# Kernel tuning notes

Measured on AMD Instinct MI355X. Metric: run time of the kernel, lower is better.

## Reference

```python
import jax, jax.numpy as jnp
import numpy as np

B, S, E, H = 2, 2048, 1024, 16
D = E // H  # head_dim
SCALE = 1.0 / np.sqrt(D)


def rope_tables(seq_len, dim, dtype=jnp.float32):
    # matches RotaryEmbedding: inv_freq over even indices, emb = cat([freqs, freqs])
    inv_freq = 1.0 / (10000.0 ** (jnp.arange(0, dim, 2, dtype=dtype) / dim))
    t = jnp.arange(seq_len, dtype=dtype)
    freqs = t[:, None] * inv_freq[None, :]          # [S, D/2]
    emb = jnp.concatenate([freqs, freqs], axis=-1)  # [S, D]
    return jnp.cos(emb)[None, None], jnp.sin(emb)[None, None]  # [1,1,S,D]


def apply_rope(x, cos, sin):
    # x: [B,H,S,D]; interleaved rotate exactly as the torch code:
    # x2 = stack([-x[...,1::2], x[...,0::2]], -1).reshape_as(x)
    x2 = jnp.stack([-x[..., 1::2], x[..., 0::2]], axis=-1).reshape(x.shape)
    return x * cos + x2 * sin


def setup_inputs() -> dict:
    key = jax.random.key(0)
    ks = jax.random.split(key, 12)
    std = 1.0 / np.sqrt(E)
    inp = {
        "query": jax.random.normal(ks[0], (B, S, E), jnp.float32),
        "key": jax.random.normal(ks[1], (B, S, E), jnp.float32),
        "value": jax.random.normal(ks[2], (B, S, E), jnp.float32),
        "mask": jnp.ones((B, S), jnp.int32),
        "Wq": jax.random.normal(ks[3], (E, E), jnp.float32) * std,
        "bq": jax.random.normal(ks[4], (E,), jnp.float32) * std,
        "Wk": jax.random.normal(ks[5], (E, E), jnp.float32) * std,
        "bk": jax.random.normal(ks[6], (E,), jnp.float32) * std,
        "Wv": jax.random.normal(ks[7], (E, E), jnp.float32) * std,
        "bv": jax.random.normal(ks[8], (E,), jnp.float32) * std,
        "Wo": jax.random.normal(ks[9], (E, E), jnp.float32) * std,
        "bo": jax.random.normal(ks[10], (E,), jnp.float32) * std,
    }
    return inp


def reference(query, key, value, mask, Wq, bq, Wk, bk, Wv, bv, Wo, bo):
    b, sq, _ = query.shape
    sk = key.shape[1]
    # linear projections (torch Linear: x @ W.T + b), split into heads [B,H,S,D]
    Q = (query @ Wq.T + bq).reshape(b, sq, H, D).transpose(0, 2, 1, 3)
    K = (key @ Wk.T + bk).reshape(b, sk, H, D).transpose(0, 2, 1, 3)
    V = (value @ Wv.T + bv).reshape(b, sk, H, D).transpose(0, 2, 1, 3)
    cos_q, sin_q = rope_tables(sq, D)
    cos_k, sin_k = rope_tables(sk, D)
    Q = apply_rope(Q, cos_q, sin_q)
    K = apply_rope(K, cos_k, sin_k)
    scores = jnp.einsum("bhqd,bhkd->bhqk", Q, K) * SCALE
    neg_inf = jnp.finfo(scores.dtype).min
    scores = jnp.where(mask[:, None, None, :] == 0, neg_inf, scores)
    attn = jax.nn.softmax(scores, axis=-1)
    # dropout omitted (deterministic reference / eval mode)
    out = jnp.einsum("bhqk,bhkd->bhqd", attn, V)
    out = out.transpose(0, 2, 1, 3).reshape(b, sq, E)
    return out @ Wo.T + bo
```

## Files before the change

### kernel.cpp

```cpp
#include <hip/hip_runtime.h>
#include <stdint.h>

typedef unsigned short u16;
typedef __bf16 bf16x8 __attribute__((ext_vector_type(8)));
typedef float f32x4 __attribute__((ext_vector_type(4)));
typedef float f32x2 __attribute__((ext_vector_type(2)));
typedef u16 u16x4v __attribute__((ext_vector_type(4)));

#define DI __device__ __forceinline__

constexpr int BB = 2, SS = 2048, EE = 1024, HH = 16, DD = 64;
constexpr int MROWS = BB * SS;
constexpr int KDIM = 1024, NDIM = 1024;

constexpr float FM = 12.0f;
constexpr float MNEG = -30000.f;

DI u16 f2bf(float f) {
  uint32_t u = __float_as_uint(f);
  return (u16)((u + 0x7FFFu + ((u >> 16) & 1u)) >> 16);
}
DI float bf2f(u16 h) { return __uint_as_float(((uint32_t)h) << 16); }

DI uint32_t cvtpk_bf16(float a, float b) {
  uint32_t r;
  asm("v_cvt_pk_bf16_f32 %0, %1, %2" : "=v"(r) : "v"(a), "v"(b));
  return r;
}

DI void cp16(const void* g, void* lds) {
  __builtin_amdgcn_global_load_lds((const __attribute__((address_space(1))) void*)g,
                                   (__attribute__((address_space(3))) void*)lds, 16, 0, 0);
}

DI f32x4 mfma16(bf16x8 a, bf16x8 b, f32x4 c) {
  return __builtin_amdgcn_mfma_f32_16x16x32_bf16(a, b, c, 0, 0, 0);
}

__global__ __launch_bounds__(256) void prep_cast(
    const float* __restrict__ q, const float* __restrict__ k, const float* __restrict__ v,
    const float* __restrict__ wq, const float* __restrict__ wk, const float* __restrict__ wv,
    const float* __restrict__ wo, const int* __restrict__ mask,
    u16* __restrict__ qb, u16* __restrict__ kb, u16* __restrict__ vb,
    u16* __restrict__ wqb, u16* __restrict__ wkb, u16* __restrict__ wvb,
    u16* __restrict__ wob, float* __restrict__ csT, float* __restrict__ mfl) {
  constexpr size_t SZI = (size_t)MROWS * EE;
  constexpr size_t SZW = (size_t)EE * EE;
  const int t = blockIdx.x * 256 + threadIdx.x;
  if (t < SS * 64) {
    const int s = t >> 6, d = t & 63, j = d & 31;
    const float ang = (float)s * exp2f(-(float)j * 0.4152410118f);
    float2 cs; cs.x = cosf(ang); cs.y = sinf(ang);
    ((float2*)csT)[t] = cs;
    if (t < BB * SS) mfl[t] = mask[t] ? -FM : MNEG;
  }
  const size_t g = ((size_t)blockIdx.x * 256 + threadIdx.x) * 4;
  const float* src; u16* dst; size_t o;
  if (g < SZI)          { src = q; dst = qb; o = g; }
  else if (g < 2 * SZI) { src = k; dst = kb; o = g - SZI; }
  else if (g < 3 * SZI) { src = v; dst = vb; o = g - 2 * SZI; }
  else {
    size_t t2 = g - 3 * SZI;
    int wi = (int)(t2 / SZW);
    o = t2 - (size_t)(wi < 4 ? wi : 3) * SZW;
    src = wi == 0 ? wq : wi == 1 ? wk : wi == 2 ? wv : wo;
    dst = wi == 0 ? wqb : wi == 1 ? wkb : wi == 2 ? wvb : wob;
  }
  const float4 f = *(const float4*)(src + o);
  u16x4v hv;
  hv[0] = f2bf(f.x); hv[1] = f2bf(f.y); hv[2] = f2bf(f.z); hv[3] = f2bf(f.w);
  *(u16x4v*)(dst + o) = hv;
}

__global__ __launch_bounds__(256) void gemm_qkv(
    const u16* __restrict__ qb, const u16* __restrict__ kb, const u16* __restrict__ vb,
    const u16* __restrict__ wqb, const u16* __restrict__ wkb, const u16* __restrict__ wvb,
    const float* __restrict__ bq, const float* __restrict__ bk, const float* __restrict__ bv,
    u16* __restrict__ Qp, u16* __restrict__ Kp, u16* __restrict__ Vtg,
    const float* __restrict__ csT) {
  __shared__ alignas(16) u16 sA[2][128 * 64];
  __shared__ alignas(16) u16 sB[2][128 * 64];
  const int flat = blockIdx.y * 8 + blockIdx.x;
  const int swz = (flat & 7) * 96 + (flat >> 3);
  const int bx = swz & 7, by = swz >> 3;

  const int tsel = by >> 5;
  const bool vtr = (tsel == 2);
  const u16* A    = tsel == 0 ? wqb : tsel == 1 ? wkb : vb;
  const u16* Bm   = tsel == 0 ? qb  : tsel == 1 ? kb  : wvb;
  const float* bias = tsel == 0 ? bq : tsel == 1 ? bk : bv;

  const int fBase = bx * 128;
  const int tBase = (by & 31) * 128;
  const int aBase = vtr ? tBase : fBase;
  const int bBase = vtr ? fBase : tBase;
  const int tid = threadIdx.x;
  const int lane = tid & 63, w = tid >> 6;
  const int quad = lane >> 4, l16 = lane & 15;
  const int wr = w >> 1, wc = w & 1;

  size_t aSrc[4], bSrc[4];
  int dOff[4];
#pragma unroll
  for (int j = 0; j < 4; ++j) {
    const int c = tid + j * 256;
    const int row = c >> 3, sl = c & 7;
    const size_t off = (size_t)row * KDIM + ((sl ^ (row & 7)) * 8);
    aSrc[j] = (size_t)aBase * KDIM + off;
    bSrc[j] = (size_t)bBase * KDIM + off;
    dOff[j] = c * 8;
  }

  f32x4 acc[4][4];
#pragma unroll
  for (int mi = 0; mi < 4; ++mi)
#pragma unroll
    for (int ni = 0; ni < 4; ++ni)
#pragma unroll
      for (int e = 0; e < 4; ++e) acc[mi][ni][e] = 0.f;

  const int arow = wr * 64 + l16, brow = wc * 64 + l16;

  auto stage = [&](int k0, int bi) {
#pragma unroll
    for (int j = 0; j < 4; ++j) {
      cp16(A + aSrc[j] + k0, &sA[bi][dOff[j]]);
      cp16(Bm + bSrc[j] + k0, &sB[bi][dOff[j]]);
    }
  };

  stage(0, 0);
  __syncthreads();
  int buf = 0;
  for (int k0 = 0; k0 < KDIM; k0 += 64) {
    if (k0 + 64 < KDIM) stage(k0 + 64, buf ^ 1);
    __builtin_amdgcn_s_setprio(1);
#pragma unroll
    for (int h = 0; h < 2; ++h) {
      bf16x8 af[4], bf[4];
#pragma unroll
      for (int i = 0; i < 4; ++i) {
        const int ar = arow + i * 16, br = brow + i * 16;
        af[i] = *(const bf16x8*)&sA[buf][ar * 64 + (((h * 4 + quad) ^ (ar & 7)) << 3)];
        bf[i] = *(const bf16x8*)&sB[buf][br * 64 + (((h * 4 + quad) ^ (br & 7)) << 3)];
      }
#pragma unroll
      for (int mi = 0; mi < 4; ++mi)
#pragma unroll
        for (int ni = 0; ni < 4; ++ni)
          acc[mi][ni] = mfma16(af[mi], bf[ni], acc[mi][ni]);
    }
    __builtin_amdgcn_s_setprio(0);
    __syncthreads();
    buf ^= 1;
  }

  if (!vtr) {
    u16* C = tsel == 0 ? Qp : Kp;
#pragma unroll
    for (int mi = 0; mi < 4; ++mi) {
      const int fm = fBase + wr * 64 + mi * 16 + quad * 4;
      const float4 b4 = *(const float4*)&bias[fm];
      const int d0 = fm & 63;
#pragma unroll
      for (int ni = 0; ni < 4; ++ni) {
        const int t = tBase + wc * 64 + ni * 16 + l16;
        const int srow = t & (SS - 1);
        const float* cs = &csT[(size_t)((srow << 6) + d0) * 2];
        const float4 cs01 = *(const float4*)cs;
        const float4 cs23 = *(const float4*)(cs + 4);
        const float v0 = acc[mi][ni][0] + b4.x;
        const float v1 = acc[mi][ni][1] + b4.y;
        const float v2 = acc[mi][ni][2] + b4.z;
        const float v3 = acc[mi][ni][3] + b4.w;
        const float o0 = v0 * cs01.x - v1 * cs01.y;
        const float o1 = v1 * cs01.z + v0 * cs01.w;
        const float o2 = v2 * cs23.x - v3 * cs23.y;
        const float o3 = v3 * cs23.z + v2 * cs23.w;
        uint2 pk;
        pk.x = cvtpk_bf16(o0, o1);
        pk.y = cvtpk_bf16(o2, o3);
        *(uint2*)&C[(size_t)t * NDIM + fm] = pk;
      }
    }
  } else {
#pragma unroll
    for (int ni = 0; ni < 4; ++ni) {
      const int f = fBase + wc * 64 + ni * 16 + l16;
      const int h = f >> 6, d = f & 63;
      const float bb = bias[f];
#pragma unroll
      for (int mi = 0; mi < 4; ++mi) {
        const int t0 = tBase + wr * 64 + mi * 16 + quad * 4;
        const int b = t0 >> 11, s0 = t0 & (SS - 1);
        const int sp0 = (s0 & ~31) | (((s0 >> 2) & 3) << 3) | (((s0 >> 4) & 1) << 2);
        uint2 pk;
        pk.x = cvtpk_bf16(acc[mi][ni][0] + bb, acc[mi][ni][1] + bb);
        pk.y = cvtpk_bf16(acc[mi][ni][2] + bb, acc[mi][ni][3] + bb);
        *(uint2*)&Vtg[((size_t)((b * 16 + h) * 64 + d)) * SS + sp0] = pk;
      }
    }
  }
}

__global__ __launch_bounds__(512, 4) void attn_kernel(
    const u16* __restrict__ Qp, const u16* __restrict__ Kp, const u16* __restrict__ Vtg,
    const float* __restrict__ mfl, u16* __restrict__ Oh) {
  __shared__ alignas(16) u16 sm[36864];
  const int flat = blockIdx.y * 16 + blockIdx.x;
  const int swz = (flat & 7) * 64 + (flat >> 3);
  const int bqx = swz & 15, bh = swz >> 4;

  const int tid = threadIdx.x, lane = tid & 63, w = tid >> 6;
  const int quad = lane >> 4, l16 = lane & 15;
  const int b = bh >> 4, h = bh & 15;
  const int q0 = bqx * 128 + (w & 3) * 32;
  const int grp = w >> 2, wl = w & 3;
  const u16* Qb = Qp + (size_t)b * SS * EE + h * DD;
  const u16* Kb = Kp + (size_t)b * SS * EE + h * DD;
  const u16* Vb = Vtg + (size_t)bh * DD * SS;
  constexpr float C1 = 0.18033688011112042f;
  float* smask = (float*)&sm[32768];

  bf16x8 qf[2][2];
#pragma unroll
  for (int qi = 0; qi < 2; ++qi)
#pragma unroll
    for (int ks = 0; ks < 2; ++ks)
      qf[qi][ks] = *(const bf16x8*)(Qb + (size_t)(q0 + qi * 16 + l16) * EE + ks * 32 + quad * 8);

  f32x4 oacc[2][4];
#pragma unroll
  for (int qi = 0; qi < 2; ++qi)
#pragma unroll
    for (int nd = 0; nd < 4; ++nd)
#pragma unroll
      for (int e = 0; e < 4; ++e) oacc[qi][nd][e] = 0.f;
  f32x2 sum2[2];
  sum2[0] = {0.f, 0.f}; sum2[1] = {0.f, 0.f};

  const int gtid = tid & 255;

  auto stage = [&](int w_, int bi) {
    const int key0 = w_ * 128 + grp * 64;
    u16* dK = &sm[grp * 16384 + bi * 4096];
    u16* dV = &sm[grp * 16384 + 8192 + bi * 4096];
#pragma unroll
    for (int i = 0; i < 2; ++i) {
      const int c = i * 256 + gtid;
      const int key = c >> 3, sl = c & 7;
      cp16(Kb + (size_t)(key0 + key) * EE + ((sl ^ (key & 7)) * 8), &dK[c * 8]);
    }
#pragma unroll
    for (int i = 0; i < 2; ++i) {
      const int c = i * 256 + gtid;
      const int d = c >> 3, sl = c & 7;
      cp16(Vb + (size_t)d * SS + key0 + ((sl ^ (d & 7)) * 8), &dV[c * 8]);
    }
  };

  auto compute = [&](int w_, int bi) {
    const int key0 = w_ * 128 + grp * 64;
    const u16* sK_ = &sm[grp * 16384 + bi * 4096];
    const u16* sV_ = &sm[grp * 16384 + 8192 + bi * 4096];
    f32x4 sacc[2][4];
#pragma unroll
    for (int qi = 0; qi < 2; ++qi)
#pragma unroll
      for (int ni = 0; ni < 4; ++ni)
#pragma unroll
        for (int e = 0; e < 4; ++e) sacc[qi][ni][e] = 0.f;
    __builtin_amdgcn_s_setprio(1);
#pragma unroll
    for (int ks = 0; ks < 2; ++ks)
#pragma unroll
      for (int ni = 0; ni < 4; ++ni) {
        const int row = ni * 16 + l16;
        const bf16x8 kf = *(const bf16x8*)&sK_[row * 64 + (((ks * 4 + quad) ^ (l16 & 7)) << 3)];
#pragma unroll
        for (int qi = 0; qi < 2; ++qi)
          sacc[qi][ni] = mfma16(kf, qf[qi][ks], sacc[qi][ni]);
      }
    __builtin_amdgcn_s_setprio(0);

    f32x2 mh01[4], mh23[4];
#pragma unroll
    for (int ni = 0; ni < 4; ++ni) {
      const int kb4 = key0 + ni * 16 + quad * 4;
      mh01[ni] = *(const f32x2*)&smask[kb4];
      mh23[ni] = *(const f32x2*)&smask[kb4 + 2];
    }

    uint32_t pw32[2][2][4];
#pragma unroll
    for (int qi = 0; qi < 2; ++qi)
#pragma unroll
      for (int ni = 0; ni < 4; ++ni) {
        f32x2 t01, t23;
        t01.x = sacc[qi][ni][0]; t01.y = sacc[qi][ni][1];
        t23.x = sacc[qi][ni][2]; t23.y = sacc[qi][ni][3];
        t01 = t01 * C1 + mh01[ni];
        t23 = t23 * C1 + mh23[ni];
        f32x2 p01, p23;
        p01.x = __builtin_amdgcn_exp2f(t01.x); p01.y = __builtin_amdgcn_exp2f(t01.y);
        p23.x = __builtin_amdgcn_exp2f(t23.x); p23.y = __builtin_amdgcn_exp2f(t23.y);
        sum2[qi] += p01;
        sum2[qi] += p23;
        const int k2 = ni >> 1, j2 = (ni & 1) * 2;
        pw32[qi][k2][j2]     = cvtpk_bf16(p01.x, p01.y);
        pw32[qi][k2][j2 + 1] = cvtpk_bf16(p23.x, p23.y);
      }

    __builtin_amdgcn_s_setprio(1);
#pragma unroll
    for (int k2 = 0; k2 < 2; ++k2) {
      union { uint32_t u[4]; bf16x8 v; } pf[2];
#pragma unroll
      for (int qi = 0; qi < 2; ++qi)
#pragma unroll
        for (int j = 0; j < 4; ++j) pf[qi].u[j] = pw32[qi][k2][j];
#pragma unroll
      for (int nd = 0; nd < 4; ++nd) {
        const int row = nd * 16 + l16;
        const bf16x8 vf = *(const bf16x8*)&sV_[row * 64 + (((k2 * 4 + quad) ^ (l16 & 7)) << 3)];
#pragma unroll
        for (int qi = 0; qi < 2; ++qi)
          oacc[qi][nd] = mfma16(pf[qi].v, vf, oacc[qi][nd]);
      }
    }
    __builtin_amdgcn_s_setprio(0);
  };

  stage(0, 0);
  cp16(mfl + (size_t)b * SS + tid * 4, &sm[32768 + tid * 8]);
  __syncthreads();

  for (int w_ = 0; w_ < 16; ++w_) {
    if (w_ + 1 < 16) stage(w_ + 1, (w_ + 1) & 1);
    compute(w_, w_ & 1);
    __syncthreads();
  }

  float lg[2];
#pragma unroll
  for (int qi = 0; qi < 2; ++qi) {
    float s = sum2[qi].x + sum2[qi].y;
    s += __shfl_xor(s, 16, 64);
    s += __shfl_xor(s, 32, 64);
    lg[qi] = s;
  }

  float* sO = (float*)&sm[0];
  float* l0 = smask;
  if (grp == 0) {
#pragma unroll
    for (int qi = 0; qi < 2; ++qi)
#pragma unroll
      for (int nd = 0; nd < 4; ++nd)
#pragma unroll
        for (int e = 0; e < 4; ++e) {
          const int q = wl * 32 + qi * 16 + quad * 4 + e;
          sO[q * 65 + nd * 16 + l16] = oacc[qi][nd][e];
        }
    if (quad == 0) {
      l0[wl * 32 + l16] = lg[0];
      l0[wl * 32 + 16 + l16] = lg[1];
    }
  }
  __syncthreads();
  if (grp == 1) {
    float linv[2];
#pragma unroll
    for (int qi = 0; qi < 2; ++qi) {
      const float lt = l0[wl * 32 + qi * 16 + l16] + lg[qi];
      linv[qi] = lt > 0.f ? 1.0f / lt : 0.f;
    }
#pragma unroll
    for (int qi = 0; qi < 2; ++qi)
#pragma unroll
      for (int r = 0; r < 4; ++r) {
        const float li = __shfl(linv[qi], quad * 4 + r, 16);
        const int q = wl * 32 + qi * 16 + quad * 4 + r;
        const size_t row = (size_t)(b * SS + bqx * 128 + q) * EE + h * DD;
#pragma unroll
        for (int nd = 0; nd < 4; ++nd) {
          const int d = nd * 16 + l16;
          Oh[row + d] = f2bf((sO[q * 65 + d] + oacc[qi][nd][r]) * li);
        }
      }
  }
}

__global__ __launch_bounds__(256) void gemm_out(
    const u16* __restrict__ Ab, const u16* __restrict__ Bb,
    const float* __restrict__ bias, float* __restrict__ Cout) {
  __shared__ alignas(16) u16 sA[2][128 * 64];
  __shared__ alignas(16) u16 sB[2][64 * 64];
  const int flat = blockIdx.y * 16 + blockIdx.x;
  const int swz = (flat & 7) * 64 + (flat >> 3);
  const int bx = swz & 15, by = swz >> 4;

  const int rowBase = by * 128;
  const int colBase = bx * 64;
  const int tid = threadIdx.x;
  const int lane = tid & 63, w = tid >> 6;
  const int quad = lane >> 4, l16 = lane & 15;
  const int wr = w >> 1, wc = w & 1;

  size_t aSrc[4]; int aOff[4];
  size_t bSrc[2]; int bOff[2];
#pragma unroll
  for (int j = 0; j < 4; ++j) {
    const int c = tid + j * 256;
    const int row = c >> 3, sl = c & 7;
    aSrc[j] = (size_t)(rowBase + row) * KDIM + ((sl ^ (row & 7)) * 8);
    aOff[j] = c * 8;
  }
#pragma unroll
  for (int j = 0; j < 2; ++j) {
    const int c = tid + j * 256;
    const int row = c >> 3, sl = c & 7;
    bSrc[j] = (size_t)(colBase + row) * KDIM + ((sl ^ (row & 7)) * 8);
    bOff[j] = c * 8;
  }

  f32x4 acc[4][2];
#pragma unroll
  for (int mi = 0; mi < 4; ++mi)
#pragma unroll
    for (int ni = 0; ni < 2; ++ni)
#pragma unroll
      for (int e = 0; e < 4; ++e) acc[mi][ni][e] = 0.f;

  const int arow = wr * 64 + l16, brow = wc * 32 + l16;

  auto stage = [&](int k0, int bi) {
#pragma unroll
    for (int j = 0; j < 4; ++j) cp16(Ab + aSrc[j] + k0, &sA[bi][aOff[j]]);
#pragma unroll
    for (int j = 0; j < 2; ++j) cp16(Bb + bSrc[j] + k0, &sB[bi][bOff[j]]);
  };

  stage(0, 0);
  __syncthreads();
  int buf = 0;
  for (int k0 = 0; k0 < KDIM; k0 += 64) {
    if (k0 + 64 < KDIM) stage(k0 + 64, buf ^ 1);
    __builtin_amdgcn_s_setprio(1);
#pragma unroll
    for (int h = 0; h < 2; ++h) {
      bf16x8 af[4], bf[2];
#pragma unroll
      for (int i = 0; i < 4; ++i) {
        const int ar = arow + i * 16;
        af[i] = *(const bf16x8*)&sA[buf][ar * 64 + (((h * 4 + quad) ^ (ar & 7)) << 3)];
      }
#pragma unroll
      for (int i = 0; i < 2; ++i) {
        const int br = brow + i * 16;
        bf[i] = *(const bf16x8*)&sB[buf][br * 64 + (((h * 4 + quad) ^ (br & 7)) << 3)];
      }
#pragma unroll
      for (int mi = 0; mi < 4; ++mi)
#pragma unroll
        for (int ni = 0; ni < 2; ++ni)
          acc[mi][ni] = mfma16(af[mi], bf[ni], acc[mi][ni]);
    }
    __builtin_amdgcn_s_setprio(0);
    __syncthreads();
    buf ^= 1;
  }

#pragma unroll
  for (int mi = 0; mi < 4; ++mi) {
    const int rb = rowBase + wr * 64 + mi * 16 + quad * 4;
#pragma unroll
    for (int ni = 0; ni < 2; ++ni) {
      const int col = colBase + wc * 32 + ni * 16 + l16;
      const float bb = bias[col];
#pragma unroll
      for (int r = 0; r < 4; ++r)
        Cout[(size_t)(rb + r) * NDIM + col] = acc[mi][ni][r] + bb;
    }
  }
}

extern "C" void kernel_launch(void* const* d_in, const int* in_sizes, int n_in,
                              void* d_out, int out_size, void* d_ws, size_t ws_size,
                              hipStream_t stream) {
  const float* q    = (const float*)d_in[0];
  const float* k    = (const float*)d_in[1];
  const float* v    = (const float*)d_in[2];
  const int*   mask = (const int*)d_in[3];
  const float* Wq = (const float*)d_in[4];
  const float* bq = (const float*)d_in[5];
  const float* Wk = (const float*)d_in[6];
  const float* bk = (const float*)d_in[7];
  const float* Wv = (const float*)d_in[8];
  const float* bv = (const float*)d_in[9];
  const float* Wo = (const float*)d_in[10];
  const float* bo = (const float*)d_in[11];
  float* out = (float*)d_out;
  char* ws = (char*)d_ws;
  constexpr size_t MB = 1024 * 1024;
  u16* qb  = (u16*)(ws + 0 * MB);
  u16* kb  = (u16*)(ws + 8 * MB);
  u16* vb  = (u16*)(ws + 16 * MB);
  u16* wqb = (u16*)(ws + 24 * MB);
  u16* wkb = (u16*)(ws + 26 * MB);
  u16* wvb = (u16*)(ws + 28 * MB);
  u16* wob = (u16*)(ws + 30 * MB);
  u16* Qp  = (u16*)(ws + 32 * MB);
  u16* Kp  = (u16*)(ws + 40 * MB);
  u16* Vtg = (u16*)(ws + 48 * MB);
  u16* oh  = (u16*)(ws + 56 * MB);
  float* csT = (float*)(ws + 64 * MB);
  float* mfl = out;

  prep_cast<<<16384, 256, 0, stream>>>(q, k, v, Wq, Wk, Wv, Wo, mask,
                                       qb, kb, vb, wqb, wkb, wvb, wob, csT, mfl);
  gemm_qkv<<<dim3(8, 96), 256, 0, stream>>>(qb, kb, vb, wqb, wkb, wvb,
                                            bq, bk, bv, Qp, Kp, Vtg, csT);
  attn_kernel<<<dim3(16, 32), 512, 0, stream>>>(Qp, Kp, Vtg, mfl, oh);
  gemm_out<<<dim3(16, 32), 256, 0, stream>>>(oh, wob, bo, out);
}
```

Baseline: 217.2 us.

## Fuse fp32-to-bf16 activation cast into QKV GEMM loads

The prep kernel now casts only the weights and builds the RoPE and mask tables. The fp32 activation casts move into gemm_qkv, which loads fp32 query/key/value tiles into registers, converts them with v_cvt_pk_bf16, and writes them to LDS after the MFMA phase, while weights still use async global-to-LDS copies. This drops a full write and reread of the three bf16 activation copies. In exchange the GEMM reads twice the activation bytes per tile, needs more registers, and does register-staged LDS writes on the critical path.

```diff
diff --git a/kernel.cpp b/kernel.cpp
--- a/kernel.cpp
+++ b/kernel.cpp
@@ -20,7 +20,6 @@
   uint32_t u = __float_as_uint(f);
   return (u16)((u + 0x7FFFu + ((u >> 16) & 1u)) >> 16);
 }
-DI float bf2f(u16 h) { return __uint_as_float(((uint32_t)h) << 16); }
 
 DI uint32_t cvtpk_bf16(float a, float b) {
   uint32_t r;
@@ -37,15 +36,12 @@
   return __builtin_amdgcn_mfma_f32_16x16x32_bf16(a, b, c, 0, 0, 0);
 }
 
-__global__ __launch_bounds__(256) void prep_cast(
-    const float* __restrict__ q, const float* __restrict__ k, const float* __restrict__ v,
-    const float* __restrict__ wq, const float* __restrict__ wk, const float* __restrict__ wv,
-    const float* __restrict__ wo, const int* __restrict__ mask,
-    u16* __restrict__ qb, u16* __restrict__ kb, u16* __restrict__ vb,
+__global__ __launch_bounds__(256) void prep_w(
+    const float* __restrict__ wq, const float* __restrict__ wk,
+    const float* __restrict__ wv, const float* __restrict__ wo,
+    const int* __restrict__ mask,
     u16* __restrict__ wqb, u16* __restrict__ wkb, u16* __restrict__ wvb,
     u16* __restrict__ wob, float* __restrict__ csT, float* __restrict__ mfl) {
-  constexpr size_t SZI = (size_t)MROWS * EE;
-  constexpr size_t SZW = (size_t)EE * EE;
   const int t = blockIdx.x * 256 + threadIdx.x;
   if (t < SS * 64) {
     const int s = t >> 6, d = t & 63, j = d & 31;
@@ -54,18 +50,11 @@
     ((float2*)csT)[t] = cs;
     if (t < BB * SS) mfl[t] = mask[t] ? -FM : MNEG;
   }
-  const size_t g = ((size_t)blockIdx.x * 256 + threadIdx.x) * 4;
-  const float* src; u16* dst; size_t o;
-  if (g < SZI)          { src = q; dst = qb; o = g; }
-  else if (g < 2 * SZI) { src = k; dst = kb; o = g - SZI; }
-  else if (g < 3 * SZI) { src = v; dst = vb; o = g - 2 * SZI; }
-  else {
-    size_t t2 = g - 3 * SZI;
-    int wi = (int)(t2 / SZW);
-    o = t2 - (size_t)(wi < 4 ? wi : 3) * SZW;
-    src = wi == 0 ? wq : wi == 1 ? wk : wi == 2 ? wv : wo;
-    dst = wi == 0 ? wqb : wi == 1 ? wkb : wi == 2 ? wvb : wob;
-  }
+  const size_t g = (size_t)t * 4;
+  const int wi = (int)(g >> 20);
+  const size_t o = g & ((1u << 20) - 1);
+  const float* src = wi == 0 ? wq : wi == 1 ? wk : wi == 2 ? wv : wo;
+  u16* dst = wi == 0 ? wqb : wi == 1 ? wkb : wi == 2 ? wvb : wob;
   const float4 f = *(const float4*)(src + o);
   u16x4v hv;
   hv[0] = f2bf(f.x); hv[1] = f2bf(f.y); hv[2] = f2bf(f.z); hv[3] = f2bf(f.w);
@@ -73,41 +62,39 @@
 }
 
 __global__ __launch_bounds__(256) void gemm_qkv(
-    const u16* __restrict__ qb, const u16* __restrict__ kb, const u16* __restrict__ vb,
+    const float* __restrict__ qf, const float* __restrict__ kf, const float* __restrict__ vf,
     const u16* __restrict__ wqb, const u16* __restrict__ wkb, const u16* __restrict__ wvb,
     const float* __restrict__ bq, const float* __restrict__ bk, const float* __restrict__ bv,
     u16* __restrict__ Qp, u16* __restrict__ Kp, u16* __restrict__ Vtg,
     const float* __restrict__ csT) {
-  __shared__ alignas(16) u16 sA[2][128 * 64];
-  __shared__ alignas(16) u16 sB[2][128 * 64];
+  __shared__ alignas(16) u16 sW[2][128 * 64];
+  __shared__ alignas(16) u16 sX[2][128 * 64];
   const int flat = blockIdx.y * 8 + blockIdx.x;
   const int swz = (flat & 7) * 96 + (flat >> 3);
   const int bx = swz & 7, by = swz >> 3;
 
   const int tsel = by >> 5;
   const bool vtr = (tsel == 2);
-  const u16* A    = tsel == 0 ? wqb : tsel == 1 ? wkb : vb;
-  const u16* Bm   = tsel == 0 ? qb  : tsel == 1 ? kb  : wvb;
+  const float* Xs = tsel == 0 ? qf : tsel == 1 ? kf : vf;
+  const u16* Ws   = tsel == 0 ? wqb : tsel == 1 ? wkb : wvb;
   const float* bias = tsel == 0 ? bq : tsel == 1 ? bk : bv;
 
   const int fBase = bx * 128;
   const int tBase = (by & 31) * 128;
-  const int aBase = vtr ? tBase : fBase;
-  const int bBase = vtr ? fBase : tBase;
   const int tid = threadIdx.x;
   const int lane = tid & 63, w = tid >> 6;
   const int quad = lane >> 4, l16 = lane & 15;
   const int wr = w >> 1, wc = w & 1;
 
-  size_t aSrc[4], bSrc[4];
+  size_t wSrc[4], xSrc[4];
   int dOff[4];
 #pragma unroll
   for (int j = 0; j < 4; ++j) {
     const int c = tid + j * 256;
     const int row = c >> 3, sl = c & 7;
-    const size_t off = (size_t)row * KDIM + ((sl ^ (row & 7)) * 8);
-    aSrc[j] = (size_t)aBase * KDIM + off;
-    bSrc[j] = (size_t)bBase * KDIM + off;
+    const int g8 = (sl ^ (row & 7)) * 8;
+    wSrc[j] = (size_t)(fBase + row) * KDIM + g8;
+    xSrc[j] = (size_t)(tBase + row) * KDIM + g8;
     dOff[j] = c * 8;
   }
 
@@ -121,28 +108,50 @@
 
   const int arow = wr * 64 + l16, brow = wc * 64 + l16;
 
-  auto stage = [&](int k0, int bi) {
+  float4 xlo[4], xhi[4];
+  auto loadX = [&](int k0) {
 #pragma unroll
     for (int j = 0; j < 4; ++j) {
-      cp16(A + aSrc[j] + k0, &sA[bi][dOff[j]]);
-      cp16(Bm + bSrc[j] + k0, &sB[bi][dOff[j]]);
+      const float* p = Xs + xSrc[j] + k0;
+      xlo[j] = *(const float4*)p;
+      xhi[j] = *(const float4*)(p + 4);
     }
   };
-
-  stage(0, 0);
+  auto writeX = [&](int bi) {
+#pragma unroll
+    for (int j = 0; j < 4; ++j) {
+      uint4 wv4;
+      wv4.x = cvtpk_bf16(xlo[j].x, xlo[j].y);
+      wv4.y = cvtpk_bf16(xlo[j].z, xlo[j].w);
+      wv4.z = cvtpk_bf16(xhi[j].x, xhi[j].y);
+      wv4.w = cvtpk_bf16(xhi[j].z, xhi[j].w);
+      *(uint4*)&sX[bi][dOff[j]] = wv4;
+    }
+  };
+  auto stageW = [&](int k0, int bi) {
+#pragma unroll
+    for (int j = 0; j < 4; ++j) cp16(Ws + wSrc[j] + k0, &sW[bi][dOff[j]]);
+  };
+
+  loadX(0);
+  stageW(0, 0);
+  writeX(0);
   __syncthreads();
   int buf = 0;
   for (int k0 = 0; k0 < KDIM; k0 += 64) {
-    if (k0 + 64 < KDIM) stage(k0 + 64, buf ^ 1);
+    const bool more = (k0 + 64 < KDIM);
+    if (more) { loadX(k0 + 64); stageW(k0 + 64, buf ^ 1); }
     __builtin_amdgcn_s_setprio(1);
+    const u16* sAf = vtr ? &sX[buf][0] : &sW[buf][0];
+    const u16* sBf = vtr ? &sW[buf][0] : &sX[buf][0];
 #pragma unroll
     for (int h = 0; h < 2; ++h) {
       bf16x8 af[4], bf[4];
 #pragma unroll
       for (int i = 0; i < 4; ++i) {
         const int ar = arow + i * 16, br = brow + i * 16;
-        af[i] = *(const bf16x8*)&sA[buf][ar * 64 + (((h * 4 + quad) ^ (ar & 7)) << 3)];
-        bf[i] = *(const bf16x8*)&sB[buf][br * 64 + (((h * 4 + quad) ^ (br & 7)) << 3)];
+        af[i] = *(const bf16x8*)&sAf[ar * 64 + (((h * 4 + quad) ^ (ar & 7)) << 3)];
+        bf[i] = *(const bf16x8*)&sBf[br * 64 + (((h * 4 + quad) ^ (br & 7)) << 3)];
       }
 #pragma unroll
       for (int mi = 0; mi < 4; ++mi)
@@ -151,6 +160,7 @@
           acc[mi][ni] = mfma16(af[mi], bf[ni], acc[mi][ni]);
     }
     __builtin_amdgcn_s_setprio(0);
+    if (more) writeX(buf ^ 1);
     __syncthreads();
     buf ^= 1;
   }
@@ -503,9 +513,6 @@
   float* out = (float*)d_out;
   char* ws = (char*)d_ws;
   constexpr size_t MB = 1024 * 1024;
-  u16* qb  = (u16*)(ws + 0 * MB);
-  u16* kb  = (u16*)(ws + 8 * MB);
-  u16* vb  = (u16*)(ws + 16 * MB);
   u16* wqb = (u16*)(ws + 24 * MB);
   u16* wkb = (u16*)(ws + 26 * MB);
   u16* wvb = (u16*)(ws + 28 * MB);
@@ -517,9 +524,9 @@
   float* csT = (float*)(ws + 64 * MB);
   float* mfl = out;
 
-  prep_cast<<<16384, 256, 0, stream>>>(q, k, v, Wq, Wk, Wv, Wo, mask,
-                                       qb, kb, vb, wqb, wkb, wvb, wob, csT, mfl);
-  gemm_qkv<<<dim3(8, 96), 256, 0, stream>>>(qb, kb, vb, wqb, wkb, wvb,
+  prep_w<<<4096, 256, 0, stream>>>(Wq, Wk, Wv, Wo, mask,
+                                   wqb, wkb, wvb, wob, csT, mfl);
+  gemm_qkv<<<dim3(8, 96), 256, 0, stream>>>(q, k, v, wqb, wkb, wvb,
                                             bq, bk, bv, Qp, Kp, Vtg, csT);
   attn_kernel<<<dim3(16, 32), 512, 0, stream>>>(Qp, Kp, Vtg, mfl, oh);
   gemm_out<<<dim3(16, 32), 256, 0, stream>>>(oh, wob, bo, out);
```

After: 242.3 us. 11.5% more time.
